# Kernel tuning notes

Measured on AMD Instinct MI355X. Metric: run time of the kernel, lower is better.

Reference implementation:

```python
import jax, jax.numpy as jnp
import numpy as np

H = 512       # hidden_dim
NL = 2        # n_layers
DICT = 128    # dict_size
T_DEC = 32    # maxlen['trad']


def _gru_bidir(x, Wih, Whh, bih, bhh):
    """Bidirectional GRU layer. x: [B,L,D]; Wih: [2,3H,D]; Whh: [2,3H,H].
    Returns (y [B,L,2H], h_final [2,B,H]) with outputs time-aligned (torch semantics)."""
    Hd = Whh.shape[-1]
    Bsz = x.shape[0]

    def run_dir(d, reverse):
        gi_all = jnp.einsum('bld,gd->blg', x, Wih[d]) + bih[d]  # [B,L,3H] input gates precomputed

        def step(h, gi_t):
            gh = h @ Whh[d].T + bhh[d]
            ir, iz, inn = jnp.split(gi_t, 3, axis=-1)
            hr, hz, hn = jnp.split(gh, 3, axis=-1)
            r = jax.nn.sigmoid(ir + hr)
            z = jax.nn.sigmoid(iz + hz)
            n = jnp.tanh(inn + r * hn)
            h_new = (1.0 - z) * n + z * h
            return h_new, h_new

        h0 = jnp.zeros((Bsz, Hd), x.dtype)
        hT, ys = jax.lax.scan(step, h0, jnp.swapaxes(gi_all, 0, 1), reverse=reverse)
        return jnp.swapaxes(ys, 0, 1), hT

    yf, hf = run_dir(0, False)
    yb, hb = run_dir(1, True)
    return jnp.concatenate([yf, yb], axis=-1), jnp.stack([hf, hb], axis=0)


def _forward(x, enc_Wih0, enc_Whh0, enc_bih0, enc_bhh0,
             enc_Wih1, enc_Whh1, enc_bih1, enc_bhh1,
             emb, dec_Wih, dec_Whh, dec_bih, dec_bhh,
             Wq, bq, We2d, be2d, Wout, bout):
    B = x.shape[0]
    xt = jnp.transpose(x, (0, 2, 1))  # [B,L,2]
    y0, h0 = _gru_bidir(xt, enc_Wih0, enc_Whh0, enc_bih0, enc_bhh0)
    y1, h1 = _gru_bidir(y0, enc_Wih1, enc_Whh1, enc_bih1, enc_bhh1)
    enc_outs = y1                               # [B,L,2H]
    h = jnp.concatenate([h0, h1], axis=0)       # [2*NL,B,H], torch h ordering
    # faithful replication of torch h.view(batch_size, -1) on (2*NL,B,H)
    hflat = h.reshape(B, -1)
    hdec = (hflat @ We2d.T + be2d).reshape(NL, B, H)

    def dec_step(carry, _):
        hid, tok = carry
        xin = emb[tok]                          # [B,H]
        new_h = []
        for l in range(NL):
            hl = jnp.tanh(xin @ dec_Wih[l].T + dec_bih[l] + hid[l] @ dec_Whh[l].T + dec_bhh[l])
            new_h.append(hl)
            xin = hl
        hid = jnp.stack(new_h, axis=0)
        vec_rnn = xin                           # [B,H]
        q = vec_rnn @ Wq.T + bq                 # [B,2H]
        scores = jnp.einsum('blh,bh->bl', enc_outs, q)
        w = jax.nn.softmax(scores, axis=1)      # softmax over encoder time (dim 1)
        att = jnp.einsum('bl,blh->bh', w, enc_outs)
        logits = jnp.concatenate([vec_rnn, att], axis=-1) @ Wout.T + bout  # [B,DICT]
        tok = jnp.argmax(logits, axis=-1)       # argmax(softmax(.)) == argmax(.)
        return (hid, tok), (logits, w)

    tok0 = jnp.zeros((B,), jnp.int32)
    (hid_f, _), (logits_seq, attw_seq) = jax.lax.scan(dec_step, (hdec, tok0), None, length=T_DEC)
    vec_out = jnp.swapaxes(logits_seq, 0, 1)    # [B,T_DEC,DICT]
    att_w = jnp.swapaxes(attw_seq, 0, 1)        # [B,T_DEC,L]
    return vec_out, hid_f, att_w


def setup_inputs() -> dict:
    key = jax.random.key(0)
    ks = jax.random.split(key, 24)
    s = 0.05
    d = {
        'x': jax.random.normal(ks[0], (64, 2, 1024), jnp.float32),
        'enc_Wih0': jax.random.normal(ks[1], (2, 3 * H, 2)) * s,
        'enc_Whh0': jax.random.normal(ks[2], (2, 3 * H, H)) * s,
        'enc_bih0': jax.random.normal(ks[3], (2, 3 * H)) * s,
        'enc_bhh0': jax.random.normal(ks[4], (2, 3 * H)) * s,
        'enc_Wih1': jax.random.normal(ks[5], (2, 3 * H, 2 * H)) * s,
        'enc_Whh1': jax.random.normal(ks[6], (2, 3 * H, H)) * s,
        'enc_bih1': jax.random.normal(ks[7], (2, 3 * H)) * s,
        'enc_bhh1': jax.random.normal(ks[8], (2, 3 * H)) * s,
        'emb': jax.random.normal(ks[9], (DICT, H)) * s,
        'dec_Wih': jax.random.normal(ks[10], (NL, H, H)) * s,
        'dec_Whh': jax.random.normal(ks[11], (NL, H, H)) * s,
        'dec_bih': jax.random.normal(ks[12], (NL, H)) * s,
        'dec_bhh': jax.random.normal(ks[13], (NL, H)) * s,
        'Wq': jax.random.normal(ks[14], (2 * H, H)) * s,
        'bq': jax.random.normal(ks[15], (2 * H,)) * s,
        'We2d': jax.random.normal(ks[16], (NL * H, 2 * NL * H)) * s,
        'be2d': jax.random.normal(ks[17], (NL * H,)) * s,
        'Wout': jax.random.normal(ks[18], (DICT, 3 * H)) * s,
        'bout': jax.random.normal(ks[19], (DICT,)) * s,
    }
    return {k: v.astype(jnp.float32) for k, v in d.items()}


def reference(x, enc_Wih0, enc_Whh0, enc_bih0, enc_bhh0,
              enc_Wih1, enc_Whh1, enc_bih1, enc_bhh1,
              emb, dec_Wih, dec_Whh, dec_bih, dec_bhh,
              Wq, bq, We2d, be2d, Wout, bout):
    return _forward(x, enc_Wih0, enc_Whh0, enc_bih0, enc_bhh0,
                    enc_Wih1, enc_Whh1, enc_bih1, enc_bhh1,
                    emb, dec_Wih, dec_Whh, dec_bih, dec_bhh,
                    Wq, bq, We2d, be2d, Wout, bout)
```

## Files before the change

kernel.cpp:

```cpp
#include <hip/hip_runtime.h>
#include <math.h>

typedef float    f4 __attribute__((ext_vector_type(4)));
typedef float    f2 __attribute__((ext_vector_type(2)));
typedef _Float16 h2 __attribute__((ext_vector_type(2)));

#define GUARD_MAX (1<<22)
#define CNT_DEC   128
#define BC_DEC    160

__device__ __forceinline__ float dot4(const f4 a, const f4 b) {
  return a.x*b.x + a.y*b.y + a.z*b.z + a.w*b.w;
}
__device__ __forceinline__ float sigm(float v) { return 1.f/(1.f + expf(-v)); }

__device__ __forceinline__ float fdot2f(h2 a, h2 b, float c) {
#if __has_builtin(__builtin_amdgcn_fdot2)
  return __builtin_amdgcn_fdot2(a, b, c, false);
#else
  return c + (float)a.x*(float)b.x + (float)a.y*(float)b.y;
#endif
}

__device__ __forceinline__ float ald(const float* p) {
  unsigned u = __hip_atomic_load((const unsigned*)p, __ATOMIC_RELAXED, __HIP_MEMORY_SCOPE_SYSTEM);
  return __uint_as_float(u);
}
__device__ __forceinline__ int aldi(const int* p) {
  return __hip_atomic_load(p, __ATOMIC_RELAXED, __HIP_MEMORY_SCOPE_SYSTEM);
}
__device__ __forceinline__ f2 ald2(const float* p) {
  unsigned long long u = __hip_atomic_load((const unsigned long long*)p,
                                           __ATOMIC_RELAXED, __HIP_MEMORY_SCOPE_SYSTEM);
  f2 r; r.x = __uint_as_float((unsigned)u); r.y = __uint_as_float((unsigned)(u >> 32));
  return r;
}
__device__ __forceinline__ f4 ald4(const float* p) {
  f2 a = ald2(p), b = ald2(p + 2);
  f4 r; r.x = a.x; r.y = a.y; r.z = b.x; r.w = b.y; return r;
}
__device__ __forceinline__ void ast(float* p, float v) {
  __hip_atomic_store((unsigned*)p, __float_as_uint(v), __ATOMIC_RELAXED, __HIP_MEMORY_SCOPE_SYSTEM);
}
__device__ __forceinline__ void asti(int* p, int v) {
  __hip_atomic_store(p, v, __ATOMIC_RELAXED, __HIP_MEMORY_SCOPE_SYSTEM);
}
__device__ __forceinline__ void ast2(float* p, float a, float b) {
  unsigned long long u = (unsigned long long)__float_as_uint(a)
                       | ((unsigned long long)__float_as_uint(b) << 32);
  __hip_atomic_store((unsigned long long*)p, u, __ATOMIC_RELAXED, __HIP_MEMORY_SCOPE_SYSTEM);
}
__device__ __forceinline__ void ld8(const float* p, float* o) {
  *(f4*)&o[0] = *(const f4*)&p[0];
  *(f4*)&o[4] = *(const f4*)&p[4];
}
__device__ __forceinline__ void ld8(const _Float16* p, float* o) {
  uint4 r = *(const uint4*)p;
  const h2* hh = (const h2*)&r;
#pragma unroll
  for (int i = 0; i < 4; ++i) { o[2*i] = (float)hh[i].x; o[2*i+1] = (float)hh[i].y; }
}
__device__ __forceinline__ void atomAddF(float* p, float v) {
  __hip_atomic_fetch_add(p, v, __ATOMIC_RELAXED, __HIP_MEMORY_SCOPE_AGENT);
}
__device__ __forceinline__ void atomAddH2(_Float16* p, float lo, float hi) {
  unsigned* u = (unsigned*)p;
  unsigned old = __hip_atomic_load(u, __ATOMIC_RELAXED, __HIP_MEMORY_SCOPE_AGENT);
  for (;;) {
    h2 c = *(h2*)&old;
    h2 n; n.x = (_Float16)((float)c.x + lo); n.y = (_Float16)((float)c.y + hi);
    unsigned nv = *(unsigned*)&n;
    unsigned got = atomicCAS(u, old, nv);
    if (got == old) break;
    old = got;
  }
}

__device__ __forceinline__ void bar_wait(const int* flags, int bidx, int tgt) {
  if (threadIdx.x == 0) {
    int guard = 0;
    while (__hip_atomic_load(&flags[bidx], __ATOMIC_RELAXED, __HIP_MEMORY_SCOPE_SYSTEM) < tgt) {
      if (++guard > GUARD_MAX) break;
      __builtin_amdgcn_s_sleep(8);
    }
  }
  __syncthreads();
  asm volatile("" ::: "memory");
}
__device__ __forceinline__ void bar_arrive(int* flags, int cidx, int bidx,
                                           int nwg, int tgt) {
  asm volatile("s_waitcnt vmcnt(0)" ::: "memory");
  __syncthreads();
  if (threadIdx.x == 0) {
    const int old = __hip_atomic_fetch_add(&flags[cidx], 1, __ATOMIC_RELAXED,
                                           __HIP_MEMORY_SCOPE_AGENT);
    if (old == nwg*tgt - 1)
      __hip_atomic_store(&flags[bidx], tgt, __ATOMIC_RELAXED, __HIP_MEMORY_SCOPE_SYSTEM);
  }
}

__global__ void k_pack(const float* __restrict__ src, _Float16* __restrict__ dst,
                       int R, int KK, int rowStride, int kStride, int dOff0, int dStep) {
  const int total = 2*KK*R*2;
  for (int idx = blockIdx.x*256 + threadIdx.x; idx < total; idx += gridDim.x*256) {
    const int p   = idx & 1;
    const int row = (idx >> 1) % R;
    const int kk  = ((idx >> 1) / R) % KK;
    const int dd  = (idx >> 1) / (R*KK);
    dst[idx] = (_Float16)src[(size_t)dd*dStep + (size_t)row*rowStride
                             + (size_t)(2*kk + p)*kStride + dOff0];
  }
}
__global__ void k_packf(const float* __restrict__ src, float* __restrict__ dst) {
  const int total = 2*128*1536;
  for (int idx = blockIdx.x*256 + threadIdx.x; idx < total; idx += gridDim.x*256) {
    const int row = idx % 1536;
    const int kk  = (idx / 1536) & 127;
    const int dd  = idx / (1536*128);
    const float* s = src + (size_t)dd*786432 + (size_t)row*512 + kk*4;
    f4 v; v.x = s[0]; v.y = s[1]; v.z = s[2]; v.w = s[3];
    *(f4*)&dst[(size_t)idx*4] = v;
  }
}

template<int MODE>
__global__ __launch_bounds__(512, 1)
void k_gru(const float* __restrict__ x0, const _Float16* __restrict__ yin,
           _Float16* __restrict__ yout,
           const float* __restrict__ WhhP, const _Float16* __restrict__ WixP,
           const float* __restrict__ Wih0,
           const float* __restrict__ bih, const float* __restrict__ bhh,
           float* __restrict__ hfin, int hfin_base,
           const _Float16* __restrict__ Wqp, const _Float16* __restrict__ Upk,
           const _Float16* __restrict__ bqp,
           _Float16* __restrict__ Zp, _Float16* __restrict__ Up,
           float* __restrict__ cp)
{
  const int g    = blockIdx.x;
  const int xcd  = g & 7;
  const int d    = (xcd < 4) ? 0 : 1;
  const int idxd = (g >> 3)*4 + (xcd & 3);
  const int b0   = idxd * 2;
  const int j    = threadIdx.x;

  __shared__ float    hF[2][2][512];
  __shared__ h2       xW[MODE ? 8 : 1][MODE ? 2 : 1][MODE ? 512 : 1];
  __shared__ _Float16 hW[MODE ? 8 : 1][MODE ? 2 : 1][MODE ? 512 : 1];

  hF[0][0][j] = 0.f; hF[0][1][j] = 0.f;

  const float biR = bih[d*1536 + j],        bhR = bhh[d*1536 + j];
  const float biZ = bih[d*1536 + 512 + j],  bhZ = bhh[d*1536 + 512 + j];
  const float biN = bih[d*1536 + 1024 + j], bhN = bhh[d*1536 + 1024 + j];
  float xwR0=0,xwR1=0,xwZ0=0,xwZ1=0,xwN0=0,xwN1=0;
  if (MODE == 0) {
    xwR0 = Wih0[(d*1536 + j)*2 + 0];        xwR1 = Wih0[(d*1536 + j)*2 + 1];
    xwZ0 = Wih0[(d*1536 + 512 + j)*2 + 0];  xwZ1 = Wih0[(d*1536 + 512 + j)*2 + 1];
    xwN0 = Wih0[(d*1536 + 1024 + j)*2 + 0]; xwN1 = Wih0[(d*1536 + 1024 + j)*2 + 1];
  }
  const f4* wh = (const f4*)WhhP + (size_t)d*196608;
  const h2* wx = MODE ? (const h2*)WixP + (size_t)d*786432 : (const h2*)nullptr;
  const h2* wq = MODE ? (const h2*)Wqp + d*131072 : (const h2*)nullptr;
  const h2* wu = MODE ? (const h2*)Upk + d*32768  : (const h2*)nullptr;
  const h2* wb = MODE ? (const h2*)bqp + d*256    : (const h2*)nullptr;
  __syncthreads();

  int cur = 0;
  for (int s8 = 0; s8 < 128; ++s8) {
    float gi[8][2][3];
    if constexpr (MODE == 1) {
      for (int n = j; n < 2048; n += 512) {
        const int tw = n >> 8, b = (n >> 7) & 1, q = n & 127;
        const int t = d ? 1023 - (s8*8 + tw) : (s8*8 + tw);
        ((uint4*)&xW[tw][b][0])[q] =
            ((const uint4*)(yin + ((size_t)(b0+b)*1024 + t)*1024))[q];
      }
      __syncthreads();
#pragma unroll
      for (int tw = 0; tw < 8; ++tw)
#pragma unroll
        for (int b = 0; b < 2; ++b) { gi[tw][b][0]=0.f; gi[tw][b][1]=0.f; gi[tw][b][2]=0.f; }
#pragma unroll 4
      for (int kk = 0; kk < 512; ++kk) {
        const h2 wr = wx[kk*1536 + j];
        const h2 wz = wx[kk*1536 + 512 + j];
        const h2 wn = wx[kk*1536 + 1024 + j];
#pragma unroll
        for (int tw = 0; tw < 8; ++tw)
#pragma unroll
          for (int b = 0; b < 2; ++b) {
            const h2 xv = xW[tw][b][kk];
            gi[tw][b][0] = fdot2f(wr, xv, gi[tw][b][0]);
            gi[tw][b][1] = fdot2f(wz, xv, gi[tw][b][1]);
            gi[tw][b][2] = fdot2f(wn, xv, gi[tw][b][2]);
          }
      }
    }

#pragma unroll
    for (int tw = 0; tw < 8; ++tw) {
      const int s = s8*8 + tw;
      const int t = d ? 1023 - s : s;
      float aR[2], aZ[2], aNh[2], NI[2];
      if constexpr (MODE == 1) {
#pragma unroll
        for (int b = 0; b < 2; ++b) {
          aR[b] = gi[tw][b][0]; aZ[b] = gi[tw][b][1]; NI[b] = gi[tw][b][2] + biN;
          aNh[b] = 0.f;
        }
      } else {
#pragma unroll
        for (int b = 0; b < 2; ++b) {
          const float xa = x0[((b0+b)*2 + 0)*1024 + t];
          const float xb = x0[((b0+b)*2 + 1)*1024 + t];
          aR[b] = xa*xwR0 + xb*xwR1;
          aZ[b] = xa*xwZ0 + xb*xwZ1;
          NI[b] = xa*xwN0 + xb*xwN1 + biN;
          aNh[b] = 0.f;
        }
      }
#pragma unroll 4
      for (int kk = 0; kk < 128; ++kk) {
        const f4 w4r = wh[kk*1536 + j];
        const f4 w4z = wh[kk*1536 + 512 + j];
        const f4 w4n = wh[kk*1536 + 1024 + j];
#pragma unroll
        for (int b = 0; b < 2; ++b) {
          const f4 hv = *(const f4*)&hF[cur][b][kk*4];
          aR[b]  += dot4(w4r, hv);
          aZ[b]  += dot4(w4z, hv);
          aNh[b] += dot4(w4n, hv);
        }
      }
#pragma unroll
      for (int b = 0; b < 2; ++b) {
        const float r_ = sigm(aR[b] + biR + bhR);
        const float z_ = sigm(aZ[b] + biZ + bhZ);
        const float n_ = tanhf(NI[b] + r_*(aNh[b] + bhN));
        const float hn = (1.f - z_)*n_ + z_*hF[cur][b][j];
        hF[cur^1][b][j] = hn;
        if constexpr (MODE == 1) hW[tw][b][j] = (_Float16)hn;
        if constexpr (MODE == 0)
          yout[((size_t)(b0+b)*1024 + t)*1024 + d*512 + j] = (_Float16)hn;
        if (s == 1023) hfin[((hfin_base + d)*64 + (b0+b))*512 + j] = hn;
      }
      cur ^= 1;
      __syncthreads();
    }

    if constexpr (MODE == 1) {
      float za[8][2];
#pragma unroll
      for (int tw = 0; tw < 8; ++tw) { za[tw][0] = 0.f; za[tw][1] = 0.f; }
#pragma unroll 4
      for (int kk = 0; kk < 256; ++kk) {
        const h2 wv = wq[kk*512 + j];
#pragma unroll
        for (int tw = 0; tw < 8; ++tw)
#pragma unroll
          for (int b = 0; b < 2; ++b)
            za[tw][b] = fdot2f(wv, ((const h2*)&hW[tw][b][0])[kk], za[tw][b]);
      }
#pragma unroll
      for (int tw = 0; tw < 8; ++tw) {
        const int t = d ? 1023 - (s8*8 + tw) : (s8*8 + tw);
#pragma unroll
        for (int b = 0; b < 2; ++b) {
          const float zhi = __shfl_down(za[tw][b], 1);
          if (!(j & 1))
            atomAddH2(&Zp[((size_t)(b0+b)*1024 + t)*512 + j], za[tw][b], zhi);
        }
      }
      if (j < 128) {
        float ua[8][2];
#pragma unroll
        for (int tw = 0; tw < 8; ++tw) { ua[tw][0] = 0.f; ua[tw][1] = 0.f; }
#pragma unroll 4
        for (int kk = 0; kk < 256; ++kk) {
          const h2 wv = wu[kk*128 + j];
#pragma unroll
          for (int tw = 0; tw < 8; ++tw)
#pragma unroll
            for (int b = 0; b < 2; ++b)
              ua[tw][b] = fdot2f(wv, ((const h2*)&hW[tw][b][0])[kk], ua[tw][b]);
        }
#pragma unroll
        for (int tw = 0; tw < 8; ++tw) {
          const int t = d ? 1023 - (s8*8 + tw) : (s8*8 + tw);
#pragma unroll
          for (int b = 0; b < 2; ++b) {
            const float uhi = __shfl_down(ua[tw][b], 1);
            if (!(j & 1))
              atomAddH2(&Up[((size_t)(b0+b)*1024 + t)*128 + j], ua[tw][b], uhi);
          }
        }
      } else if (j < 192) {
        const int l = j - 128;
        float ca[8][2];
#pragma unroll
        for (int tw = 0; tw < 8; ++tw) { ca[tw][0] = 0.f; ca[tw][1] = 0.f; }
#pragma unroll
        for (int q = 0; q < 4; ++q) {
          const h2 wv = wb[l + q*64];
#pragma unroll
          for (int tw = 0; tw < 8; ++tw)
#pragma unroll
            for (int b = 0; b < 2; ++b)
              ca[tw][b] = fdot2f(wv, ((const h2*)&hW[tw][b][0])[l + q*64], ca[tw][b]);
        }
#pragma unroll
        for (int tw = 0; tw < 8; ++tw) {
          const int t = d ? 1023 - (s8*8 + tw) : (s8*8 + tw);
#pragma unroll
          for (int b = 0; b < 2; ++b) {
            float cs = ca[tw][b];
            for (int off = 1; off < 64; off <<= 1) cs += __shfl_xor(cs, off);
            if (l == 0) atomAddF(&cp[(b0+b)*1024 + t], cs);
          }
        }
      }
      __syncthreads();
    }
  }
}

__global__ __launch_bounds__(256, 1)
void k_we2d(const float* __restrict__ hfin, const float* __restrict__ We2d,
            const float* __restrict__ be2d, float* __restrict__ dech,
            int* __restrict__ tok)
{
  const int g = blockIdx.x, tid = threadIdx.x;
  const int r = tid >> 2, jl = tid & 3;
  const int j = g*4 + jl;
  const float* wr = We2d + (size_t)j*2048;
  float acc = 0.f;
  for (int c = 0; c < 2048; c += 4) {
    const int q = r*4 + (c >> 9);
    acc += dot4(*(const f4*)&hfin[((q >> 6)*64 + (q & 63))*512 + (c & 511)],
                *(const f4*)&wr[c]);
  }
  acc += be2d[j];
  const int lp = r >> 5, bb2 = 2*(r & 31) + (j >> 9), hh = j & 511;
  dech[(lp*64 + bb2)*512 + hh] = acc;
  if (g == 0 && tid < 64) tok[tid] = 0;
}

__global__ __launch_bounds__(256, 1)
void k_dec(const float* __restrict__ emb, const float* __restrict__ dWih,
           const float* __restrict__ dWhh, const float* __restrict__ dbih,
           const float* __restrict__ dbhh, const float* __restrict__ Wout,
           const float* __restrict__ bout, const _Float16* __restrict__ Zp,
           const _Float16* __restrict__ Up, const float* __restrict__ cp,
           float* __restrict__ dech, float* __restrict__ scor,
           float* __restrict__ pvU, float* __restrict__ pms,
           int* __restrict__ tok, int* __restrict__ flags,
           float* __restrict__ out)
{
  __shared__ float shmU[4][128];
  __shared__ float wms[8];
  __shared__ float shv[512];
  __shared__ float shl[128];

  const int g = blockIdx.x, tid = threadIdx.x;

  for (int s = 0; s < 32; ++s) {
    const int p = s & 1, pn = p ^ 1;
    const int tb = s*4;

    bar_wait(flags, BC_DEC, tb);
    if (g < 64) {
      const int b = tid & 63, jj = tid >> 6;
      const int tk = aldi(tok + b);
      const float* xi = emb + (size_t)tk*512;
      const float* hh = dech + ((p*2 + 0)*64 + b)*512;
#pragma unroll
      for (int o = 0; o < 2; ++o) {
        const int j = g*8 + jj + o*4;
        const float* wi = dWih + (size_t)j*512;
        const float* wh = dWhh + (size_t)j*512;
        float acc = dbih[j] + dbhh[j];
        for (int k = 0; k < 512; k += 4) {
          acc += dot4(*(const f4*)&xi[k], *(const f4*)&wi[k]);
          acc += dot4(ald4(&hh[k]), *(const f4*)&wh[k]);
        }
        ast(&dech[((pn*2 + 0)*64 + b)*512 + j], tanhf(acc));
      }
    }
    bar_arrive(flags, CNT_DEC, BC_DEC, 256, tb+1);

    bar_wait(flags, BC_DEC, tb+1);
    if (g < 64) {
      const int b = tid & 63, jj = tid >> 6;
      const float* xi = dech + ((pn*2 + 0)*64 + b)*512;
      const float* hh = dech + ((p*2 + 1)*64 + b)*512;
#pragma unroll
      for (int o = 0; o < 2; ++o) {
        const int j = g*8 + jj + o*4;
        const float* wi = dWih + (size_t)(512 + j)*512;
        const float* wh = dWhh + (size_t)(512 + j)*512;
        float acc = dbih[512 + j] + dbhh[512 + j];
        for (int k = 0; k < 512; k += 4) {
          acc += dot4(ald4(&xi[k]), *(const f4*)&wi[k]);
          acc += dot4(ald4(&hh[k]), *(const f4*)&wh[k]);
        }
        ast(&dech[((pn*2 + 1)*64 + b)*512 + j], tanhf(acc));
      }
    }
    bar_arrive(flags, CNT_DEC, BC_DEC, 256, tb+2);

    bar_wait(flags, BC_DEC, tb+2);
    {
      const int b = g >> 2, quarter = g & 3;
      const int w = tid >> 6, lane = tid & 63;
      const float* vecb = dech + ((pn*2 + 1)*64 + b)*512;
      float vr[8];
      *(f4*)&vr[0] = ald4(&vecb[lane*8]);
      *(f4*)&vr[4] = ald4(&vecb[lane*8 + 4]);
      float m = -INFINITY, ssum = 0.f, vu0 = 0.f, vu1 = 0.f;
      const int t0 = quarter*256 + w*64;
      for (int tg = 0; tg < 64; tg += 4) {
        float zz[4][8]; float cc[4]; float2 uu[4];
#pragma unroll
        for (int u = 0; u < 4; ++u) {
          const int t = t0 + tg + u;
          ld8(Zp + ((size_t)b*1024 + t)*512 + lane*8, zz[u]);
          h2 uh = ((const h2*)(Up + ((size_t)b*1024 + t)*128))[lane];
          uu[u].x = (float)uh.x; uu[u].y = (float)uh.y;
          cc[u] = cp[b*1024 + t];
        }
#pragma unroll
        for (int u = 0; u < 4; ++u) {
          float sc = 0.f;
#pragma unroll
          for (int z = 0; z < 8; ++z) sc += zz[u][z]*vr[z];
#pragma unroll
          for (int off = 1; off < 64; off <<= 1) sc += __shfl_xor(sc, off);
          sc += cc[u];
          if (lane == 0) ast(&scor[b*1024 + t0 + tg + u], sc);
          const float mn = fmaxf(m, sc);
          const float al = expf(m - mn);
          const float wt = expf(sc - mn);
          ssum = ssum*al + wt;
          vu0 = vu0*al + wt*uu[u].x;
          vu1 = vu1*al + wt*uu[u].y;
          m = mn;
        }
      }
      shmU[w][lane*2] = vu0; shmU[w][lane*2 + 1] = vu1;
      if (lane == 0) { wms[w] = m; wms[4 + w] = ssum; }
      __syncthreads();
      const float M = fmaxf(fmaxf(wms[0], wms[1]), fmaxf(wms[2], wms[3]));
      const float e0 = expf(wms[0]-M), e1 = expf(wms[1]-M),
                  e2 = expf(wms[2]-M), e3 = expf(wms[3]-M);
      const float S = e0*wms[4] + e1*wms[5] + e2*wms[6] + e3*wms[7];
      if (tid < 128)
        ast(&pvU[(b*4 + quarter)*128 + tid],
            e0*shmU[0][tid] + e1*shmU[1][tid] + e2*shmU[2][tid] + e3*shmU[3][tid]);
      if (tid == 0) ast2(&pms[(b*4+quarter)*2], M, S);
    }
    bar_arrive(flags, CNT_DEC, BC_DEC, 256, tb+3);

    bar_wait(flags, BC_DEC, tb+3);
    if (g < 64) {
      const int b = g;
      f2 ms[4];
#pragma unroll
      for (int c = 0; c < 4; ++c) ms[c] = ald2(&pms[(b*4 + c)*2]);
      const float M = fmaxf(fmaxf(ms[0].x, ms[1].x), fmaxf(ms[2].x, ms[3].x));
      float ee[4]; float S = 0.f;
#pragma unroll
      for (int c = 0; c < 4; ++c) { ee[c] = expf(ms[c].x - M); S += ee[c]*ms[c].y; }
      const float invS = 1.f/S;
      const float* vecb = dech + ((pn*2 + 1)*64 + b)*512;
      {
        f2 v = ald2(&vecb[tid*2]);
        shv[tid*2] = v.x; shv[tid*2+1] = v.y;
      }
      __syncthreads();
      if (tid < 128) {
        const float* wr = Wout + (size_t)tid*1536;
        float acc = bout[tid];
        for (int k = 0; k < 512; k += 4)
          acc += dot4(*(const f4*)&shv[k], *(const f4*)&wr[k]);
        float att = 0.f;
#pragma unroll
        for (int c = 0; c < 4; ++c) att += ee[c]*ald(&pvU[(b*4 + c)*128 + tid]);
        acc += att * invS;
        shl[tid] = acc;
        out[(b*32 + s)*128 + tid] = acc;
      }
      __syncthreads();
      if (tid == 0) {
        float best = shl[0]; int bi = 0;
        for (int j = 1; j < 128; ++j) if (shl[j] > best) { best = shl[j]; bi = j; }
        asti(&tok[b], bi);
      }
      {
        const f4 scv = ald4(&scor[b*1024 + tid*4]);
        const int t4 = tid*4;
        out[327680 + (b*32 + s)*1024 + t4 + 0] = expf(scv.x - M)*invS;
        out[327680 + (b*32 + s)*1024 + t4 + 1] = expf(scv.y - M)*invS;
        out[327680 + (b*32 + s)*1024 + t4 + 2] = expf(scv.z - M)*invS;
        out[327680 + (b*32 + s)*1024 + t4 + 3] = expf(scv.w - M)*invS;
      }
      if (s == 31) {
        for (int u = tid; u < 1024; u += 256) {
          const int l = u >> 9, h = u & 511;
          out[262144 + (l*64 + b)*512 + h] = ald(&dech[((pn*2 + l)*64 + b)*512 + h]);
        }
      }
    }
    bar_arrive(flags, CNT_DEC, BC_DEC, 256, tb+4);
  }
}

extern "C" void kernel_launch(void* const* d_in, const int* in_sizes, int n_in,
                              void* d_out, int out_size, void* d_ws, size_t ws_size,
                              hipStream_t stream) {
  (void)in_sizes; (void)n_in;
  const float* x     = (const float*)d_in[0];
  const float* Wih0  = (const float*)d_in[1];
  const float* Whh0  = (const float*)d_in[2];
  const float* bih0  = (const float*)d_in[3];
  const float* bhh0  = (const float*)d_in[4];
  const float* Wih1  = (const float*)d_in[5];
  const float* Whh1  = (const float*)d_in[6];
  const float* bih1  = (const float*)d_in[7];
  const float* bhh1  = (const float*)d_in[8];
  const float* emb   = (const float*)d_in[9];
  const float* dWih  = (const float*)d_in[10];
  const float* dWhh  = (const float*)d_in[11];
  const float* dbih  = (const float*)d_in[12];
  const float* dbhh  = (const float*)d_in[13];
  const float* Wq    = (const float*)d_in[14];
  const float* bqv   = (const float*)d_in[15];
  const float* We2d  = (const float*)d_in[16];
  const float* be2d  = (const float*)d_in[17];
  const float* Wout  = (const float*)d_in[18];
  const float* boutv = (const float*)d_in[19];

  char* base = (char*)d_ws;
  size_t off = 0;
  auto carve = [&](size_t bytes) { size_t o = off; off += (bytes + 255) & ~(size_t)255; return o; };
  const size_t o_y0   = carve(134217728);
  const size_t o_Z    = carve(67108864);
  const size_t o_U    = carve(16777216);
  const size_t o_cp   = carve(262144);
  const size_t o_flag = carve(16384);
  const size_t o_w0h  = carve(6291456);
  const size_t o_w1h  = carve(6291456);
  const size_t o_w1x  = carve(6291456);
  const size_t o_wqp  = carve(1048576);
  const size_t o_upk  = carve(262144);
  const size_t o_bqp  = carve(2048);
  const size_t o_hfin = carve(524288);
  const size_t o_dech = carve(524288);
  const size_t o_scor = carve(262144);
  const size_t o_pvU  = carve(131072);
  const size_t o_pms  = carve(2048);
  const size_t o_tok  = carve(256);
  const size_t NEED   = off;

  if (ws_size < NEED) {
    hipMemsetAsync(d_out, 0, (size_t)out_size * 4, stream);
    return;
  }

  _Float16* y0   = (_Float16*)(base + o_y0);
  _Float16* Zp   = (_Float16*)(base + o_Z);
  _Float16* Up   = (_Float16*)(base + o_U);
  float*    cp   = (float*)(base + o_cp);
  int*      flags= (int*)(base + o_flag);
  float*    w0h  = (float*)(base + o_w0h);
  float*    w1h  = (float*)(base + o_w1h);
  _Float16* w1x  = (_Float16*)(base + o_w1x);
  _Float16* wqp  = (_Float16*)(base + o_wqp);
  _Float16* upk  = (_Float16*)(base + o_upk);
  _Float16* bqp  = (_Float16*)(base + o_bqp);
  float*    hfin = (float*)(base + o_hfin);
  float*    dech = (float*)(base + o_dech);
  float*    scor = (float*)(base + o_scor);
  float*    pvU  = (float*)(base + o_pvU);
  float*    pms  = (float*)(base + o_pms);
  int*      tok  = (int*)(base + o_tok);

  hipMemsetAsync(base + o_Z, 0, (o_flag + 16384) - o_Z, stream);

  k_packf<<<384, 256, 0, stream>>>(Whh0, w0h);
  k_packf<<<384, 256, 0, stream>>>(Whh1, w1h);
  k_pack<<<512, 256, 0, stream>>>(Wih1, w1x, 1536, 512, 1024, 1, 0, 1572864);
  k_pack<<<128, 256, 0, stream>>>(Wq,   wqp,  512, 256, 1, 512, 0, 262144);
  k_pack<<<64,  256, 0, stream>>>(Wout, upk,  128, 256, 1536, 1, 512, 512);
  k_pack<<<8,   256, 0, stream>>>(bqv,  bqp,  1,   256, 0, 1, 0, 512);

  k_gru<0><<<64, 512, 0, stream>>>(
      x, nullptr, y0, w0h, nullptr, Wih0, bih0, bhh0, hfin, 0,
      nullptr, nullptr, nullptr, nullptr, nullptr, nullptr);
  k_gru<1><<<64, 512, 0, stream>>>(
      nullptr, y0, nullptr, w1h, w1x, nullptr, bih1, bhh1, hfin, 2,
      wqp, upk, bqp, Zp, Up, cp);

  k_we2d<<<256, 256, 0, stream>>>(hfin, We2d, be2d, dech, tok);
  k_dec<<<256, 256, 0, stream>>>(emb, dWih, dWhh, dbih, dbhh, Wout, boutv,
                                 Zp, Up, cp, dech, scor, pvU, pms, tok,
                                 flags, (float*)d_out);
}
```

Measured before the change: 98.85 ms.

## Double GRU block threads to split recurrent K-reduction and batch work

The GRU kernels now launch 1024 threads per block instead of 512. The two halves split the recurrent matvec along K and combine partial sums through new shared buffers. After the reduction, each half owns one batch element for the gate math and half of the timesteps for the Wq/Wout projections. Nontemporal loads and stores are added for streamed weights and activations. The change targets latency per recurrent step, at the cost of an extra barrier per step and more register pressure under 1024-thread launch bounds.

New measurement: 104.6 ms. +5.8%, slower.

```diff
diff --git a/kernel.cpp b/kernel.cpp
--- a/kernel.cpp
+++ b/kernel.cpp
@@ -4,6 +4,7 @@
 typedef float    f4 __attribute__((ext_vector_type(4)));
 typedef float    f2 __attribute__((ext_vector_type(2)));
 typedef _Float16 h2 __attribute__((ext_vector_type(2)));
+typedef unsigned u4 __attribute__((ext_vector_type(4)));
 
 #define GUARD_MAX (1<<22)
 #define CNT_DEC   128
@@ -21,6 +22,9 @@
   return c + (float)a.x*(float)b.x + (float)a.y*(float)b.y;
 #endif
 }
+__device__ __forceinline__ h2 ntld(const h2* p) { return __builtin_nontemporal_load(p); }
+__device__ __forceinline__ u4 ntld4u(const u4* p) { return __builtin_nontemporal_load(p); }
+__device__ __forceinline__ void ntst(_Float16* p, _Float16 v) { __builtin_nontemporal_store(v, p); }
 
 __device__ __forceinline__ float ald(const float* p) {
   unsigned u = __hip_atomic_load((const unsigned*)p, __ATOMIC_RELAXED, __HIP_MEMORY_SCOPE_SYSTEM);
@@ -55,7 +59,7 @@
   *(f4*)&o[4] = *(const f4*)&p[4];
 }
 __device__ __forceinline__ void ld8(const _Float16* p, float* o) {
-  uint4 r = *(const uint4*)p;
+  u4 r = *(const u4*)p;
   const h2* hh = (const h2*)&r;
 #pragma unroll
   for (int i = 0; i < 4; ++i) { o[2*i] = (float)hh[i].x; o[2*i+1] = (float)hh[i].y; }
@@ -124,7 +128,7 @@
 }
 
 template<int MODE>
-__global__ __launch_bounds__(512, 1)
+__global__ __launch_bounds__(1024, 1)
 void k_gru(const float* __restrict__ x0, const _Float16* __restrict__ yin,
            _Float16* __restrict__ yout,
            const float* __restrict__ WhhP, const _Float16* __restrict__ WixP,
@@ -141,22 +145,27 @@
   const int d    = (xcd < 4) ? 0 : 1;
   const int idxd = (g >> 3)*4 + (xcd & 3);
   const int b0   = idxd * 2;
-  const int j    = threadIdx.x;
+  const int tid  = threadIdx.x;
+  const int jj   = tid & 511;
+  const int half = tid >> 9;
 
   __shared__ float    hF[2][2][512];
+  __shared__ float    pR[2][2][512];
+  __shared__ float    pZ[2][2][512];
+  __shared__ float    pN[2][2][512];
   __shared__ h2       xW[MODE ? 8 : 1][MODE ? 2 : 1][MODE ? 512 : 1];
   __shared__ _Float16 hW[MODE ? 8 : 1][MODE ? 2 : 1][MODE ? 512 : 1];
 
-  hF[0][0][j] = 0.f; hF[0][1][j] = 0.f;
-
-  const float biR = bih[d*1536 + j],        bhR = bhh[d*1536 + j];
-  const float biZ = bih[d*1536 + 512 + j],  bhZ = bhh[d*1536 + 512 + j];
-  const float biN = bih[d*1536 + 1024 + j], bhN = bhh[d*1536 + 1024 + j];
+  hF[0][half][jj] = 0.f;
+
+  const float biR = bih[d*1536 + jj],        bhR = bhh[d*1536 + jj];
+  const float biZ = bih[d*1536 + 512 + jj],  bhZ = bhh[d*1536 + 512 + jj];
+  const float biN = bih[d*1536 + 1024 + jj], bhN = bhh[d*1536 + 1024 + jj];
   float xwR0=0,xwR1=0,xwZ0=0,xwZ1=0,xwN0=0,xwN1=0;
   if (MODE == 0) {
-    xwR0 = Wih0[(d*1536 + j)*2 + 0];        xwR1 = Wih0[(d*1536 + j)*2 + 1];
-    xwZ0 = Wih0[(d*1536 + 512 + j)*2 + 0];  xwZ1 = Wih0[(d*1536 + 512 + j)*2 + 1];
-    xwN0 = Wih0[(d*1536 + 1024 + j)*2 + 0]; xwN1 = Wih0[(d*1536 + 1024 + j)*2 + 1];
+    xwR0 = Wih0[(d*1536 + jj)*2 + 0];        xwR1 = Wih0[(d*1536 + jj)*2 + 1];
+    xwZ0 = Wih0[(d*1536 + 512 + jj)*2 + 0];  xwZ1 = Wih0[(d*1536 + 512 + jj)*2 + 1];
+    xwN0 = Wih0[(d*1536 + 1024 + jj)*2 + 0]; xwN1 = Wih0[(d*1536 + 1024 + jj)*2 + 1];
   }
   const f4* wh = (const f4*)WhhP + (size_t)d*196608;
   const h2* wx = MODE ? (const h2*)WixP + (size_t)d*786432 : (const h2*)nullptr;
@@ -167,33 +176,29 @@
 
   int cur = 0;
   for (int s8 = 0; s8 < 128; ++s8) {
-    float gi[8][2][3];
+    float gi[MODE ? 8 : 1][3];
     if constexpr (MODE == 1) {
-      for (int n = j; n < 2048; n += 512) {
+      for (int n = tid; n < 2048; n += 1024) {
         const int tw = n >> 8, b = (n >> 7) & 1, q = n & 127;
         const int t = d ? 1023 - (s8*8 + tw) : (s8*8 + tw);
-        ((uint4*)&xW[tw][b][0])[q] =
-            ((const uint4*)(yin + ((size_t)(b0+b)*1024 + t)*1024))[q];
+        ((u4*)&xW[tw][b][0])[q] =
+            ntld4u(((const u4*)(yin + ((size_t)(b0+b)*1024 + t)*1024)) + q);
       }
       __syncthreads();
 #pragma unroll
-      for (int tw = 0; tw < 8; ++tw)
-#pragma unroll
-        for (int b = 0; b < 2; ++b) { gi[tw][b][0]=0.f; gi[tw][b][1]=0.f; gi[tw][b][2]=0.f; }
+      for (int tw = 0; tw < 8; ++tw) { gi[tw][0]=0.f; gi[tw][1]=0.f; gi[tw][2]=0.f; }
 #pragma unroll 4
       for (int kk = 0; kk < 512; ++kk) {
-        const h2 wr = wx[kk*1536 + j];
-        const h2 wz = wx[kk*1536 + 512 + j];
-        const h2 wn = wx[kk*1536 + 1024 + j];
-#pragma unroll
-        for (int tw = 0; tw < 8; ++tw)
-#pragma unroll
-          for (int b = 0; b < 2; ++b) {
-            const h2 xv = xW[tw][b][kk];
-            gi[tw][b][0] = fdot2f(wr, xv, gi[tw][b][0]);
-            gi[tw][b][1] = fdot2f(wz, xv, gi[tw][b][1]);
-            gi[tw][b][2] = fdot2f(wn, xv, gi[tw][b][2]);
-          }
+        const h2 wr = ntld(&wx[kk*1536 + jj]);
+        const h2 wz = ntld(&wx[kk*1536 + 512 + jj]);
+        const h2 wn = ntld(&wx[kk*1536 + 1024 + jj]);
+#pragma unroll
+        for (int tw = 0; tw < 8; ++tw) {
+          const h2 xv = xW[tw][half][kk];
+          gi[tw][0] = fdot2f(wr, xv, gi[tw][0]);
+          gi[tw][1] = fdot2f(wz, xv, gi[tw][1]);
+          gi[tw][2] = fdot2f(wn, xv, gi[tw][2]);
+        }
       }
     }
 
@@ -201,119 +206,121 @@
     for (int tw = 0; tw < 8; ++tw) {
       const int s = s8*8 + tw;
       const int t = d ? 1023 - s : s;
-      float aR[2], aZ[2], aNh[2], NI[2];
-      if constexpr (MODE == 1) {
-#pragma unroll
-        for (int b = 0; b < 2; ++b) {
-          aR[b] = gi[tw][b][0]; aZ[b] = gi[tw][b][1]; NI[b] = gi[tw][b][2] + biN;
-          aNh[b] = 0.f;
-        }
-      } else {
-#pragma unroll
-        for (int b = 0; b < 2; ++b) {
-          const float xa = x0[((b0+b)*2 + 0)*1024 + t];
-          const float xb = x0[((b0+b)*2 + 1)*1024 + t];
-          aR[b] = xa*xwR0 + xb*xwR1;
-          aZ[b] = xa*xwZ0 + xb*xwZ1;
-          NI[b] = xa*xwN0 + xb*xwN1 + biN;
-          aNh[b] = 0.f;
-        }
-      }
+      float aR[2] = {0.f, 0.f}, aZ[2] = {0.f, 0.f}, aN[2] = {0.f, 0.f};
 #pragma unroll 4
-      for (int kk = 0; kk < 128; ++kk) {
-        const f4 w4r = wh[kk*1536 + j];
-        const f4 w4z = wh[kk*1536 + 512 + j];
-        const f4 w4n = wh[kk*1536 + 1024 + j];
+      for (int kq = 0; kq < 64; ++kq) {
+        const int kk = half*64 + kq;
+        const f4 w4r = wh[kk*1536 + jj];
+        const f4 w4z = wh[kk*1536 + 512 + jj];
+        const f4 w4n = wh[kk*1536 + 1024 + jj];
 #pragma unroll
         for (int b = 0; b < 2; ++b) {
           const f4 hv = *(const f4*)&hF[cur][b][kk*4];
-          aR[b]  += dot4(w4r, hv);
-          aZ[b]  += dot4(w4z, hv);
-          aNh[b] += dot4(w4n, hv);
-        }
-      }
-#pragma unroll
-      for (int b = 0; b < 2; ++b) {
-        const float r_ = sigm(aR[b] + biR + bhR);
-        const float z_ = sigm(aZ[b] + biZ + bhZ);
-        const float n_ = tanhf(NI[b] + r_*(aNh[b] + bhN));
-        const float hn = (1.f - z_)*n_ + z_*hF[cur][b][j];
-        hF[cur^1][b][j] = hn;
-        if constexpr (MODE == 1) hW[tw][b][j] = (_Float16)hn;
+          aR[b] += dot4(w4r, hv);
+          aZ[b] += dot4(w4z, hv);
+          aN[b] += dot4(w4n, hv);
+        }
+      }
+      pR[half][0][jj] = aR[0]; pR[half][1][jj] = aR[1];
+      pZ[half][0][jj] = aZ[0]; pZ[half][1][jj] = aZ[1];
+      pN[half][0][jj] = aN[0]; pN[half][1][jj] = aN[1];
+      __syncthreads();
+      {
+        float aRc = pR[0][half][jj] + pR[1][half][jj];
+        float aZc = pZ[0][half][jj] + pZ[1][half][jj];
+        float aNc = pN[0][half][jj] + pN[1][half][jj];
+        float NI;
+        if constexpr (MODE == 1) {
+          NI = gi[tw][2] + biN; aRc += gi[tw][0]; aZc += gi[tw][1];
+        } else {
+          const float xa = x0[((b0+half)*2 + 0)*1024 + t];
+          const float xb = x0[((b0+half)*2 + 1)*1024 + t];
+          NI = xa*xwN0 + xb*xwN1 + biN;
+          aRc += xa*xwR0 + xb*xwR1;
+          aZc += xa*xwZ0 + xb*xwZ1;
+        }
+        const float r_ = sigm(aRc + biR + bhR);
+        const float z_ = sigm(aZc + biZ + bhZ);
+        const float n_ = tanhf(NI + r_*(aNc + bhN));
+        const float hn = (1.f - z_)*n_ + z_*hF[cur][half][jj];
+        hF[cur^1][half][jj] = hn;
+        if constexpr (MODE == 1) hW[tw][half][jj] = (_Float16)hn;
         if constexpr (MODE == 0)
-          yout[((size_t)(b0+b)*1024 + t)*1024 + d*512 + j] = (_Float16)hn;
-        if (s == 1023) hfin[((hfin_base + d)*64 + (b0+b))*512 + j] = hn;
+          ntst(&yout[((size_t)(b0+half)*1024 + t)*1024 + d*512 + jj], (_Float16)hn);
+        if (s == 1023) hfin[((hfin_base + d)*64 + (b0+half))*512 + jj] = hn;
       }
       cur ^= 1;
       __syncthreads();
     }
 
     if constexpr (MODE == 1) {
-      float za[8][2];
-#pragma unroll
-      for (int tw = 0; tw < 8; ++tw) { za[tw][0] = 0.f; za[tw][1] = 0.f; }
-#pragma unroll 4
-      for (int kk = 0; kk < 256; ++kk) {
-        const h2 wv = wq[kk*512 + j];
-#pragma unroll
-        for (int tw = 0; tw < 8; ++tw)
-#pragma unroll
-          for (int b = 0; b < 2; ++b)
-            za[tw][b] = fdot2f(wv, ((const h2*)&hW[tw][b][0])[kk], za[tw][b]);
-      }
-#pragma unroll
-      for (int tw = 0; tw < 8; ++tw) {
-        const int t = d ? 1023 - (s8*8 + tw) : (s8*8 + tw);
-#pragma unroll
-        for (int b = 0; b < 2; ++b) {
-          const float zhi = __shfl_down(za[tw][b], 1);
-          if (!(j & 1))
-            atomAddH2(&Zp[((size_t)(b0+b)*1024 + t)*512 + j], za[tw][b], zhi);
-        }
-      }
-      if (j < 128) {
-        float ua[8][2];
-#pragma unroll
-        for (int tw = 0; tw < 8; ++tw) { ua[tw][0] = 0.f; ua[tw][1] = 0.f; }
+      {
+        float za[4][2];
+#pragma unroll
+        for (int ti = 0; ti < 4; ++ti) { za[ti][0] = 0.f; za[ti][1] = 0.f; }
 #pragma unroll 4
         for (int kk = 0; kk < 256; ++kk) {
-          const h2 wv = wu[kk*128 + j];
-#pragma unroll
-          for (int tw = 0; tw < 8; ++tw)
+          const h2 wv = wq[kk*512 + jj];
+#pragma unroll
+          for (int ti = 0; ti < 4; ++ti)
 #pragma unroll
             for (int b = 0; b < 2; ++b)
-              ua[tw][b] = fdot2f(wv, ((const h2*)&hW[tw][b][0])[kk], ua[tw][b]);
-        }
-#pragma unroll
-        for (int tw = 0; tw < 8; ++tw) {
-          const int t = d ? 1023 - (s8*8 + tw) : (s8*8 + tw);
+              za[ti][b] = fdot2f(wv, ((const h2*)&hW[half*4 + ti][b][0])[kk], za[ti][b]);
+        }
+#pragma unroll
+        for (int ti = 0; ti < 4; ++ti) {
+          const int t = d ? 1023 - (s8*8 + half*4 + ti) : (s8*8 + half*4 + ti);
 #pragma unroll
           for (int b = 0; b < 2; ++b) {
-            const float uhi = __shfl_down(ua[tw][b], 1);
-            if (!(j & 1))
-              atomAddH2(&Up[((size_t)(b0+b)*1024 + t)*128 + j], ua[tw][b], uhi);
+            const float zhi = __shfl_down(za[ti][b], 1);
+            if (!(jj & 1))
+              atomAddH2(&Zp[((size_t)(b0+b)*1024 + t)*512 + jj], za[ti][b], zhi);
           }
         }
-      } else if (j < 192) {
-        const int l = j - 128;
-        float ca[8][2];
-#pragma unroll
-        for (int tw = 0; tw < 8; ++tw) { ca[tw][0] = 0.f; ca[tw][1] = 0.f; }
+      }
+      if (jj < 128) {
+        float ua[4][2];
+#pragma unroll
+        for (int ti = 0; ti < 4; ++ti) { ua[ti][0] = 0.f; ua[ti][1] = 0.f; }
+#pragma unroll 4
+        for (int kk = 0; kk < 256; ++kk) {
+          const h2 wv = wu[kk*128 + jj];
+#pragma unroll
+          for (int ti = 0; ti < 4; ++ti)
+#pragma unroll
+            for (int b = 0; b < 2; ++b)
+              ua[ti][b] = fdot2f(wv, ((const h2*)&hW[half*4 + ti][b][0])[kk], ua[ti][b]);
+        }
+#pragma unroll
+        for (int ti = 0; ti < 4; ++ti) {
+          const int t = d ? 1023 - (s8*8 + half*4 + ti) : (s8*8 + half*4 + ti);
+#pragma unroll
+          for (int b = 0; b < 2; ++b) {
+            const float uhi = __shfl_down(ua[ti][b], 1);
+            if (!(jj & 1))
+              atomAddH2(&Up[((size_t)(b0+b)*1024 + t)*128 + jj], ua[ti][b], uhi);
+          }
+        }
+      } else if (jj < 192) {
+        const int l = jj - 128;
+        float ca[4][2];
+#pragma unroll
+        for (int ti = 0; ti < 4; ++ti) { ca[ti][0] = 0.f; ca[ti][1] = 0.f; }
 #pragma unroll
         for (int q = 0; q < 4; ++q) {
           const h2 wv = wb[l + q*64];
 #pragma unroll
-          for (int tw = 0; tw < 8; ++tw)
+          for (int ti = 0; ti < 4; ++ti)
 #pragma unroll
             for (int b = 0; b < 2; ++b)
-              ca[tw][b] = fdot2f(wv, ((const h2*)&hW[tw][b][0])[l + q*64], ca[tw][b]);
-        }
-#pragma unroll
-        for (int tw = 0; tw < 8; ++tw) {
-          const int t = d ? 1023 - (s8*8 + tw) : (s8*8 + tw);
+              ca[ti][b] = fdot2f(wv, ((const h2*)&hW[half*4 + ti][b][0])[l + q*64], ca[ti][b]);
+        }
+#pragma unroll
+        for (int ti = 0; ti < 4; ++ti) {
+          const int t = d ? 1023 - (s8*8 + half*4 + ti) : (s8*8 + half*4 + ti);
 #pragma unroll
           for (int b = 0; b < 2; ++b) {
-            float cs = ca[tw][b];
+            float cs = ca[ti][b];
             for (int off = 1; off < 64; off <<= 1) cs += __shfl_xor(cs, off);
             if (l == 0) atomAddF(&cp[(b0+b)*1024 + t], cs);
           }
@@ -593,10 +600,10 @@
   k_pack<<<64,  256, 0, stream>>>(Wout, upk,  128, 256, 1536, 1, 512, 512);
   k_pack<<<8,   256, 0, stream>>>(bqv,  bqp,  1,   256, 0, 1, 0, 512);
 
-  k_gru<0><<<64, 512, 0, stream>>>(
+  k_gru<0><<<64, 1024, 0, stream>>>(
       x, nullptr, y0, w0h, nullptr, Wih0, bih0, bhh0, hfin, 0,
       nullptr, nullptr, nullptr, nullptr, nullptr, nullptr);
-  k_gru<1><<<64, 512, 0, stream>>>(
+  k_gru<1><<<64, 1024, 0, stream>>>(
       nullptr, y0, nullptr, w1h, w1x, nullptr, bih1, bhh1, hfin, 2,
       wqp, upk, bqp, Zp, Up, cp);
 
```
